# Performance work log

Measured on AMD Instinct MI355X. Metric: run time of the kernel, lower is better.

## Reference

```python
import jax, jax.numpy as jnp
import numpy as np

H = 128      # hidden_dim
HEADS = 4
HD = H // HEADS
B, S, D, A, I = 64, 512, 64, 3, 13


def layernorm(x, g, b, eps=1e-5):
    m = x.mean(-1, keepdims=True)
    v = ((x - m) ** 2).mean(-1, keepdims=True)
    return g * (x - m) / jnp.sqrt(v + eps) + b


def setup_inputs() -> dict:
    key = jax.random.key(0)
    ks = jax.random.split(key, 12)
    rn = lambda k, shp, s=0.05: jax.random.normal(k, shp, jnp.float32) * s
    return {
        "x": jax.random.normal(ks[0], (B, S, D), jnp.float32),
        "info": jax.random.normal(ks[1], (B, I), jnp.float32),
        "W_cell": rn(ks[2], (4 * H, D + H)), "b_cell": jnp.zeros(4 * H, jnp.float32),
        "Wqkv": rn(ks[3], (3 * H, H)), "bqkv": jnp.zeros(3 * H, jnp.float32),
        "Wo": rn(ks[4], (H, H)), "bo": jnp.zeros(H, jnp.float32),
        "ln_g": jnp.ones(H, jnp.float32), "ln_b": jnp.zeros(H, jnp.float32),
        "Wa1": rn(ks[5], (128, H + I)), "ba1": jnp.zeros(128, jnp.float32),
        "lna_g": jnp.ones(128, jnp.float32), "lna_b": jnp.zeros(128, jnp.float32),
        "Wa2": rn(ks[6], (A, 128)), "ba2": jnp.zeros(A, jnp.float32),
        "Wc1": rn(ks[7], (128, H + I)), "bc1": jnp.zeros(128, jnp.float32),
        "lnc_g": jnp.ones(128, jnp.float32), "lnc_b": jnp.zeros(128, jnp.float32),
        "Wc2": rn(ks[8], (1, 128)), "bc2": jnp.zeros(1, jnp.float32),
    }


def reference(x, info, W_cell, b_cell, Wqkv, bqkv, Wo, bo, ln_g, ln_b,
              Wa1, ba1, lna_g, lna_b, Wa2, ba2, Wc1, bc1, lnc_g, lnc_b, Wc2, bc2):
    Bx, Sx, _ = x.shape
    h0 = jnp.zeros((Bx, H), x.dtype)
    c0 = jnp.zeros((Bx, H), x.dtype)
    n0 = jnp.ones((Bx, H), x.dtype)

    def step(carry, xt):
        h, c, n = carry
        gates = jnp.concatenate([xt, h], -1) @ W_cell.T + b_cell
        i, f, o, z = jnp.split(gates, 4, axis=-1)
        i = jnp.exp(jnp.clip(i, -5.0, 5.0))
        f = jnp.exp(jnp.clip(f, -5.0, 5.0))
        c = jnp.clip(f * c + i * jnp.tanh(z), -1e6, 1e6)
        n = jnp.clip(f * n + i, 1e-6, 1e6)
        h = jnp.nan_to_num(jax.nn.sigmoid(o) * (c / n), nan=0.0, posinf=0.0, neginf=0.0)
        return (h, c, n), h

    _, hs = jax.lax.scan(step, (h0, c0, n0), jnp.swapaxes(x, 0, 1))  # (S,B,H)
    seq_h = jnp.swapaxes(hs, 0, 1)  # (B,S,H)

    # MultiheadAttention (self-attn, batch_first, shared in_proj)
    qkv = seq_h @ Wqkv.T + bqkv
    q, k, v = jnp.split(qkv, 3, -1)
    split_heads = lambda t: t.reshape(Bx, Sx, HEADS, HD).transpose(0, 2, 1, 3)
    q, k, v = split_heads(q), split_heads(k), split_heads(v)
    scores = jnp.einsum('bhqd,bhkd->bhqk', q, k) / np.sqrt(HD).astype(np.float32)
    attn = jax.nn.softmax(scores, axis=-1)
    av = jnp.einsum('bhqk,bhkd->bhqd', attn, v).transpose(0, 2, 1, 3).reshape(Bx, Sx, H)
    attn_out = av @ Wo.T + bo
    context = layernorm(seq_h + attn_out, ln_g, ln_b).mean(axis=1)  # (B,H)

    comb = jnp.concatenate([context, info], -1)  # (B, H+I)
    action_probs = jax.nn.softmax(
        jax.nn.relu(layernorm(comb @ Wa1.T + ba1, lna_g, lna_b)) @ Wa2.T + ba2, axis=-1)
    value = jax.nn.relu(layernorm(comb @ Wc1.T + bc1, lnc_g, lnc_b)) @ Wc2.T + bc2
    return (action_probs, value)
```

## Files before the change

kernel.cpp:

```cpp
#include <hip/hip_runtime.h>

typedef unsigned short ushort_t;
typedef unsigned int uint_t;

__device__ __forceinline__ float bflo(uint_t u){ union{uint_t i;float f;}v; v.i=u<<16; return v.f; }
__device__ __forceinline__ float bfhi(uint_t u){ union{uint_t i;float f;}v; v.i=u&0xffff0000u; return v.f; }
__device__ __forceinline__ float bfu(ushort_t u){ union{uint_t i;float f;}v; v.i=((uint_t)u)<<16; return v.f; }
__device__ __forceinline__ ushort_t f2b(float f){
  union{float f;uint_t i;}v; v.f=f;
  uint_t r = v.i + 0x7fffu + ((v.i>>16)&1u);
  return (ushort_t)(r>>16);
}
__device__ __forceinline__ void ld8bf(const ushort_t* p, float* w){
  uint4 u = *(const uint4*)p;
  w[0]=bflo(u.x); w[1]=bfhi(u.x); w[2]=bflo(u.y); w[3]=bfhi(u.y);
  w[4]=bflo(u.z); w[5]=bfhi(u.z); w[6]=bflo(u.w); w[7]=bfhi(u.w);
}
__device__ __forceinline__ void cvt8(uint4 u, float* d){
  d[0]=bflo(u.x); d[1]=bfhi(u.x); d[2]=bflo(u.y); d[3]=bfhi(u.y);
  d[4]=bflo(u.z); d[5]=bfhi(u.z); d[6]=bflo(u.w); d[7]=bfhi(u.w);
}
__device__ __forceinline__ float ldin(const void* p, size_t i, int isbf){
  return isbf ? bfu(((const ushort_t*)p)[i]) : ((const float*)p)[i];
}
__device__ __forceinline__ float rlane(float v, int l){
  return __uint_as_float(__builtin_amdgcn_readlane(__float_as_uint(v), l));
}

#define DOT128(acc, Wv, Bv) { float s0_=0.f,s1_=0.f,s2_=0.f,s3_=0.f; \
  _Pragma("unroll") \
  for (int k_=0;k_<128;k_+=4){ float4 h4_ = *(const float4*)&(Bv)[k_]; \
    s0_ += (Wv)[k_]*h4_.x; s1_ += (Wv)[k_+1]*h4_.y; \
    s2_ += (Wv)[k_+2]*h4_.z; s3_ += (Wv)[k_+3]*h4_.w; } \
  acc += (s0_+s1_)+(s2_+s3_); }
#define DOT64A(acc, Wv, Bv) { float s0_=0.f,s1_=0.f,s2_=0.f,s3_=0.f; \
  _Pragma("unroll") \
  for (int k_=0;k_<64;k_+=4){ float4 h4_ = *(const float4*)&(Bv)[k_]; \
    s0_ += (Wv)[k_]*h4_.x; s1_ += (Wv)[k_+1]*h4_.y; \
    s2_ += (Wv)[k_+2]*h4_.z; s3_ += (Wv)[k_+3]*h4_.w; } \
  acc += (s0_+s1_)+(s2_+s3_); }

typedef __attribute__((ext_vector_type(8))) short bf16x8;
typedef __attribute__((ext_vector_type(8))) _Float16 f16x8;
typedef __attribute__((ext_vector_type(4))) float f32x4;
__device__ __forceinline__ bf16x8 bcast8(uint4 u){ return __builtin_bit_cast(bf16x8, u); }
__device__ __forceinline__ f16x8  hcast8(uint4 u){ return __builtin_bit_cast(f16x8, u); }
__device__ __forceinline__ bf16x8 cvt8bf(const float* p){
  float4 a = *(const float4*)p; float4 b = *(const float4*)(p+4);
  uint4 u;
  u.x = (uint_t)f2b(a.x) | ((uint_t)f2b(a.y)<<16);
  u.y = (uint_t)f2b(a.z) | ((uint_t)f2b(a.w)<<16);
  u.z = (uint_t)f2b(b.x) | ((uint_t)f2b(b.y)<<16);
  u.w = (uint_t)f2b(b.z) | ((uint_t)f2b(b.w)<<16);
  return bcast8(u);
}
__device__ __forceinline__ void cvt8hl(const float* p, bf16x8* hi, bf16x8* lo){
  float v[8];
  *(float4*)&v[0] = *(const float4*)p;
  *(float4*)&v[4] = *(const float4*)(p+4);
  ushort_t h[8], l[8];
  #pragma unroll
  for (int j=0;j<8;++j){ h[j] = f2b(v[j]); l[j] = f2b(v[j] - bfu(h[j])); }
  uint4 uh = { (uint_t)h[0]|((uint_t)h[1]<<16), (uint_t)h[2]|((uint_t)h[3]<<16),
               (uint_t)h[4]|((uint_t)h[5]<<16), (uint_t)h[6]|((uint_t)h[7]<<16) };
  uint4 ul = { (uint_t)l[0]|((uint_t)l[1]<<16), (uint_t)l[2]|((uint_t)l[3]<<16),
               (uint_t)l[4]|((uint_t)l[5]<<16), (uint_t)l[6]|((uint_t)l[7]<<16) };
  *hi = bcast8(uh); *lo = bcast8(ul);
}
__device__ __forceinline__ ushort_t f2h(float f){
  _Float16 h = (_Float16)f;
  return __builtin_bit_cast(ushort_t, h);
}
__device__ __forceinline__ float h2f(ushort_t u){
  _Float16 h = __builtin_bit_cast(_Float16, u);
  return (float)h;
}

__global__ void k_detect(const uint_t* __restrict__ lng_raw, int* __restrict__ flag){
  if (threadIdx.x == 0) *flag = (lng_raw[0] == 0x3F803F80u) ? 1 : 0;
}

__global__ __launch_bounds__(256) void k_cvtw(const float* __restrict__ Wq,
    const float* __restrict__ Wo, const float* __restrict__ Wc,
    ushort_t* __restrict__ wqb, ushort_t* __restrict__ wob,
    ushort_t* __restrict__ wxh, ushort_t* __restrict__ wxl,
    ushort_t* __restrict__ whf, ushort_t* __restrict__ whl,
    const int* __restrict__ flag){
  if (*flag == 1) return;
  int i = blockIdx.x*256 + threadIdx.x;
  if (i < 12288){
    float4 f = ((const float4*)Wq)[i];
    uint2 u = { (uint_t)f2b(f.x) | ((uint_t)f2b(f.y)<<16),
                (uint_t)f2b(f.z) | ((uint_t)f2b(f.w)<<16) };
    ((uint2*)wqb)[i] = u;
  } else if (i < 16384){
    int k = i - 12288;
    float4 f = ((const float4*)Wo)[k];
    uint2 u = { (uint_t)f2b(f.x) | ((uint_t)f2b(f.y)<<16),
                (uint_t)f2b(f.z) | ((uint_t)f2b(f.w)<<16) };
    ((uint2*)wob)[k] = u;
  } else if (i < 24576){
    int k = i - 16384;
    int j = k >> 4, kq = (k & 15)*4;
    float4 f = *(const float4*)(Wc + (size_t)j*192 + kq);
    ushort_t h0=f2b(f.x), h1=f2b(f.y), h2=f2b(f.z), h3=f2b(f.w);
    ushort_t l0=f2b(f.x-bfu(h0)), l1=f2b(f.y-bfu(h1));
    ushort_t l2=f2b(f.z-bfu(h2)), l3=f2b(f.w-bfu(h3));
    ((uint2*)(wxh + (size_t)j*64 + kq))[0] = { (uint_t)h0|((uint_t)h1<<16), (uint_t)h2|((uint_t)h3<<16) };
    ((uint2*)(wxl + (size_t)j*64 + kq))[0] = { (uint_t)l0|((uint_t)l1<<16), (uint_t)l2|((uint_t)l3<<16) };
  } else if (i < 32768){
    int k2 = i - 24576;
    int j = k2 >> 4, kc = (k2 & 15)*8;
    const float* src = Wc + (size_t)j*192 + 64 + kc;
    ushort_t hh[8], ll[8];
    #pragma unroll
    for (int q=0;q<8;++q){
      hh[q] = f2h(src[q]);
      ll[q] = f2h(src[q] - h2f(hh[q]));
    }
    uint4 uh = { (uint_t)hh[0]|((uint_t)hh[1]<<16), (uint_t)hh[2]|((uint_t)hh[3]<<16),
                 (uint_t)hh[4]|((uint_t)hh[5]<<16), (uint_t)hh[6]|((uint_t)hh[7]<<16) };
    uint4 ul = { (uint_t)ll[0]|((uint_t)ll[1]<<16), (uint_t)ll[2]|((uint_t)ll[3]<<16),
                 (uint_t)ll[4]|((uint_t)ll[5]<<16), (uint_t)ll[6]|((uint_t)ll[7]<<16) };
    *(uint4*)(whf + (size_t)j*136 + kc) = uh;
    *(uint4*)(whl + (size_t)j*128 + kc) = ul;
  }
}

__global__ __launch_bounds__(256) void k_gx_bf(const void* __restrict__ x,
    const void* __restrict__ Wc, const void* __restrict__ bc,
    float* __restrict__ gx, const int* __restrict__ flag){
  if (*flag == 0) return;
  __shared__ float xs[2048];
  int row0 = blockIdx.x*32, t = threadIdx.x;
  {
    uint4 u = ((const uint4*)((const ushort_t*)x + (size_t)row0*64))[t];
    cvt8(u, &xs[t*8]);
  }
  __syncthreads();
  for (int pass=0; pass<2; ++pass){
    int j = t + pass*256;
    float w[64];
    const ushort_t* wr = (const ushort_t*)Wc + (size_t)j*192;
    #pragma unroll
    for (int q=0;q<8;q++) ld8bf(wr + 8*q, &w[8*q]);
    float bj = bfu(((const ushort_t*)bc)[j]);
    for (int s=0;s<32;++s){
      float acc = bj;
      DOT64A(acc, w, &xs[s*64]);
      gx[(size_t)(row0+s)*512 + j] = acc;
    }
  }
}

__global__ __launch_bounds__(256) void k_gx_f32(const float* __restrict__ x,
    const float* __restrict__ bc,
    const ushort_t* __restrict__ wxh, const ushort_t* __restrict__ wxl,
    float* __restrict__ gx, const int* __restrict__ flag){
  if (*flag == 1) return;
  int t = threadIdx.x, lane = t & 63, wave = t >> 6;
  int l16 = lane & 15, quad = lane >> 4;
  int rowb = blockIdx.x*64 + wave*16;
  const float* xp = x + (size_t)(rowb + l16)*64;
  bf16x8 xh0, xl0, xh1, xl1;
  cvt8hl(xp + quad*8,      &xh0, &xl0);
  cvt8hl(xp + 32 + quad*8, &xh1, &xl1);
  int r0 = rowb + quad*4;
  for (int ct=0; ct<32; ++ct){
    int j = ct*16 + l16;
    const ushort_t* bh = wxh + (size_t)j*64 + quad*8;
    const ushort_t* bl = wxl + (size_t)j*64 + quad*8;
    bf16x8 wh0 = bcast8(*(const uint4*)(bh));
    bf16x8 wh1 = bcast8(*(const uint4*)(bh + 32));
    bf16x8 wl0 = bcast8(*(const uint4*)(bl));
    bf16x8 wl1 = bcast8(*(const uint4*)(bl + 32));
    f32x4 acc = {0.f,0.f,0.f,0.f};
    acc = __builtin_amdgcn_mfma_f32_16x16x32_bf16(xh0, wh0, acc, 0,0,0);
    acc = __builtin_amdgcn_mfma_f32_16x16x32_bf16(xh1, wh1, acc, 0,0,0);
    acc = __builtin_amdgcn_mfma_f32_16x16x32_bf16(xh0, wl0, acc, 0,0,0);
    acc = __builtin_amdgcn_mfma_f32_16x16x32_bf16(xh1, wl1, acc, 0,0,0);
    acc = __builtin_amdgcn_mfma_f32_16x16x32_bf16(xl0, wh0, acc, 0,0,0);
    acc = __builtin_amdgcn_mfma_f32_16x16x32_bf16(xl1, wh1, acc, 0,0,0);
    float bj = bc[j];
    #pragma unroll
    for (int r=0;r<4;++r)
      gx[(size_t)(r0+r)*512 + j] = acc[r] + bj;
  }
}

__global__ __attribute__((amdgpu_flat_work_group_size(1024,1024), amdgpu_waves_per_eu(4,4)))
void k_rec_hl(const ushort_t* __restrict__ whf,
    const ushort_t* __restrict__ whl,
    const float* __restrict__ gx, float* __restrict__ seq_h,
    const int* __restrict__ flag){
  if (*flag == 1) return;
  int b = blockIdx.x, t = threadIdx.x;
  int lane = t & 63, wv = t >> 6, l16 = lane & 15, quad = lane >> 4;
  __shared__ ushort_t wlds[512*136];
  __shared__ float gs[512];
  __shared__ ushort_t hh[128], hl[128];
  {
    const uint4* src = (const uint4*)whf;
    uint4* dst = (uint4*)wlds;
    for (int i=t; i<8704; i+=1024) dst[i] = src[i];
  }
  if (t < 128){ hh[t] = (ushort_t)0; hl[t] = (ushort_t)0; }
  const float* gxb = gx + (size_t)b*512*512;
  float g0=0.f,g1=0.f,g2=0.f,g3=0.f;
  float c = 0.f, n = 1.f;
  if (t < 128){
    g0 = gxb[t]; g1 = gxb[128+t]; g2 = gxb[256+t]; g3 = gxb[384+t];
  }
  float* shout = seq_h + (size_t)b*512*128;
  __syncthreads();
  const int ct0 = 2*wv, ct1 = 2*wv+1;
  const ushort_t* w0 = wlds + (ct0*16 + l16)*136 + quad*8;
  const ushort_t* w1 = wlds + (ct1*16 + l16)*136 + quad*8;
  const ushort_t* v0 = whl + (size_t)(ct0*16 + l16)*128 + quad*8;
  const ushort_t* v1 = whl + (size_t)(ct1*16 + l16)*128 + quad*8;
  uint4 U00 = *(const uint4*)(w0),    U01 = *(const uint4*)(w0+32);
  uint4 U02 = *(const uint4*)(w0+64), U03 = *(const uint4*)(w0+96);
  uint4 U10 = *(const uint4*)(w1),    U11 = *(const uint4*)(w1+32);
  uint4 U12 = *(const uint4*)(w1+64), U13 = *(const uint4*)(w1+96);
  uint4 V00 = *(const uint4*)(v0),    V01 = *(const uint4*)(v0+32);
  uint4 V02 = *(const uint4*)(v0+64), V03 = *(const uint4*)(v0+96);
  uint4 V10 = *(const uint4*)(v1),    V11 = *(const uint4*)(v1+32);
  uint4 V12 = *(const uint4*)(v1+64), V13 = *(const uint4*)(v1+96);
#define UPIN(U) asm volatile("" : "+v"(U.x), "+v"(U.y), "+v"(U.z), "+v"(U.w));
  UPIN(U00) UPIN(U01) UPIN(U02) UPIN(U03)
  UPIN(U10) UPIN(U11) UPIN(U12) UPIN(U13)
  UPIN(V00) UPIN(V01) UPIN(V02) UPIN(V03)
  UPIN(V10) UPIN(V11) UPIN(V12) UPIN(V13)
#undef UPIN
  const uint4 zero4 = {0u,0u,0u,0u};
  for (int ts=0; ts<512; ++ts){
    uint4 a0 = zero4, a1 = zero4, a2 = zero4, a3 = zero4;
    if (l16 == 0){
      a0 = *(const uint4*)&hh[quad*8];
      a1 = *(const uint4*)&hh[32+quad*8];
      a2 = *(const uint4*)&hh[64+quad*8];
      a3 = *(const uint4*)&hh[96+quad*8];
    } else if (l16 == 1){
      a0 = *(const uint4*)&hl[quad*8];
      a1 = *(const uint4*)&hl[32+quad*8];
      a2 = *(const uint4*)&hl[64+quad*8];
      a3 = *(const uint4*)&hl[96+quad*8];
    }
    f16x8 A0 = hcast8(a0), A1 = hcast8(a1), A2 = hcast8(a2), A3 = hcast8(a3);
    f32x4 s0 = {0.f,0.f,0.f,0.f}, s1 = {0.f,0.f,0.f,0.f};
    s0 = __builtin_amdgcn_mfma_f32_16x16x32_f16(A0, hcast8(U00), s0, 0,0,0);
    s1 = __builtin_amdgcn_mfma_f32_16x16x32_f16(A0, hcast8(U10), s1, 0,0,0);
    s0 = __builtin_amdgcn_mfma_f32_16x16x32_f16(A1, hcast8(U01), s0, 0,0,0);
    s1 = __builtin_amdgcn_mfma_f32_16x16x32_f16(A1, hcast8(U11), s1, 0,0,0);
    s0 = __builtin_amdgcn_mfma_f32_16x16x32_f16(A2, hcast8(U02), s0, 0,0,0);
    s1 = __builtin_amdgcn_mfma_f32_16x16x32_f16(A2, hcast8(U12), s1, 0,0,0);
    s0 = __builtin_amdgcn_mfma_f32_16x16x32_f16(A3, hcast8(U03), s0, 0,0,0);
    s1 = __builtin_amdgcn_mfma_f32_16x16x32_f16(A3, hcast8(U13), s1, 0,0,0);
    s0 = __builtin_amdgcn_mfma_f32_16x16x32_f16(A0, hcast8(V00), s0, 0,0,0);
    s1 = __builtin_amdgcn_mfma_f32_16x16x32_f16(A0, hcast8(V10), s1, 0,0,0);
    s0 = __builtin_amdgcn_mfma_f32_16x16x32_f16(A1, hcast8(V01), s0, 0,0,0);
    s1 = __builtin_amdgcn_mfma_f32_16x16x32_f16(A1, hcast8(V11), s1, 0,0,0);
    s0 = __builtin_amdgcn_mfma_f32_16x16x32_f16(A2, hcast8(V02), s0, 0,0,0);
    s1 = __builtin_amdgcn_mfma_f32_16x16x32_f16(A2, hcast8(V12), s1, 0,0,0);
    s0 = __builtin_amdgcn_mfma_f32_16x16x32_f16(A3, hcast8(V03), s0, 0,0,0);
    s1 = __builtin_amdgcn_mfma_f32_16x16x32_f16(A3, hcast8(V13), s1, 0,0,0);
    if (quad == 0){
      gs[ct0*16 + l16] = s0[0] + s0[1];
      gs[ct1*16 + l16] = s1[0] + s1[1];
    }
    __syncthreads();
    if (t < 128){
      float gi = gs[t]     + g0;
      float gf = gs[128+t] + g1;
      float go = gs[256+t] + g2;
      float gz = gs[384+t] + g3;
      if (ts+1 < 512){
        const float* gn = gxb + (size_t)(ts+1)*512;
        g0 = gn[t]; g1 = gn[128+t]; g2 = gn[256+t]; g3 = gn[384+t];
      }
      float ii = __expf(fminf(fmaxf(gi,-5.f),5.f));
      float ff = __expf(fminf(fmaxf(gf,-5.f),5.f));
      float e2 = __expf(2.f*gz);
      float zt = 1.f - 2.f/(e2+1.f);
      c = fminf(fmaxf(ff*c + ii*zt, -1e6f), 1e6f);
      n = fminf(fmaxf(ff*n + ii, 1e-6f), 1e6f);
      float oo = 1.f/(1.f+__expf(-go));
      float h = oo*(c/n);
      if (!isfinite(h)) h = 0.f;
      shout[(size_t)ts*128 + t] = h;
      ushort_t hhi = f2h(h);
      hh[t] = hhi;
      hl[t] = f2h(h - h2f(hhi));
    }
    __syncthreads();
  }
}

__global__ __launch_bounds__(1024, 4) void k_rec_bf(const void* __restrict__ Wc,
    const float* __restrict__ gx, float* __restrict__ seq_h,
    const int* __restrict__ flag){
  if (*flag == 0) return;
  int b = blockIdx.x, t = threadIdx.x;
  int lane = t & 63, j = t & 511, half = t >> 9;
  __shared__ float ps[1024];
  __shared__ float hs[128];
  uint_t wu[32];
  {
    const uint4* wp = (const uint4*)((const ushort_t*)Wc + (size_t)j*192 + 64 + 64*half);
    #pragma unroll
    for (int q=0;q<8;q++){ uint4 u = wp[q];
      wu[4*q]=u.x; wu[4*q+1]=u.y; wu[4*q+2]=u.z; wu[4*q+3]=u.w; }
  }
  const float* gxb = gx + (size_t)b*512*512;
  float g0=0.f, g1=0.f;
  if (half==0){ g0 = gxb[j]; g1 = gxb[512 + j]; }
  float hreg = 0.f;
  float c = 0.f, n = 1.f;
  float* shout = seq_h + (size_t)b*512*128;
  for (int ts=0; ts<512; ++ts){
    float a0, a1=0.f, a2=0.f, a3=0.f;
    if (half==0){
      a0 = g0; g0 = g1;
      g1 = (ts+2 < 512) ? gxb[(size_t)(ts+2)*512 + j] : 0.f;
    } else a0 = 0.f;
    #pragma unroll
    for (int kk=0; kk<32; kk+=2){
      float h0v = rlane(hreg, 2*kk),   h1v = rlane(hreg, 2*kk+1);
      float h2v = rlane(hreg, 2*kk+2), h3v = rlane(hreg, 2*kk+3);
      a0 = fmaf(bflo(wu[kk]),   h0v, a0);
      a1 = fmaf(bfhi(wu[kk]),   h1v, a1);
      a2 = fmaf(bflo(wu[kk+1]), h2v, a2);
      a3 = fmaf(bfhi(wu[kk+1]), h3v, a3);
    }
    ps[t] = (a0+a1)+(a2+a3);
    __syncthreads();
    if (t < 128){
      float gi = ps[t]     + ps[512+t];
      float gf = ps[128+t] + ps[640+t];
      float go = ps[256+t] + ps[768+t];
      float gz = ps[384+t] + ps[896+t];
      float ii = __expf(fminf(fmaxf(gi,-5.f),5.f));
      float ff = __expf(fminf(fmaxf(gf,-5.f),5.f));
      float e2 = __expf(2.f*gz);
      float zt = 1.f - 2.f/(e2+1.f);
      c = fminf(fmaxf(ff*c + ii*zt, -1e6f), 1e6f);
      n = fminf(fmaxf(ff*n + ii, 1e-6f), 1e6f);
      float oo = 1.f/(1.f+__expf(-go));
      float h = oo*(c/n);
      if (!isfinite(h)) h = 0.f;
      hs[t] = h;
      shout[(size_t)ts*128 + t] = h;
    }
    __syncthreads();
    hreg = hs[(half<<6) | lane];
  }
}

__global__ __launch_bounds__(512) void k_rec_inl(const void* __restrict__ x,
    const void* __restrict__ Wc, const void* __restrict__ bc,
    float* __restrict__ seq_h, const int* __restrict__ flag){
  int isbf = *flag;
  int b = blockIdx.x, j = threadIdx.x;
  __shared__ float hs[128];
  __shared__ float gs[512];
  __shared__ float xr[4][64];
  float w[128], wx[64];
  if (isbf){
    const ushort_t* wr = (const ushort_t*)Wc + (size_t)j*192;
    #pragma unroll
    for (int q=0;q<8;q++)  ld8bf(wr + 8*q, &wx[8*q]);
    #pragma unroll
    for (int q=0;q<16;q++) ld8bf(wr + 64 + 8*q, &w[8*q]);
  } else {
    const float* wr = (const float*)Wc + (size_t)j*192;
    #pragma unroll
    for (int q=0;q<16;q++){ float4 f=*(const float4*)(wr+4*q);
      wx[4*q]=f.x; wx[4*q+1]=f.y; wx[4*q+2]=f.z; wx[4*q+3]=f.w; }
    #pragma unroll
    for (int q=0;q<32;q++){ float4 f=*(const float4*)(wr+64+4*q);
      w[4*q]=f.x; w[4*q+1]=f.y; w[4*q+2]=f.z; w[4*q+3]=f.w; }
  }
  float bj = ldin(bc, j, isbf);
  float c = 0.f, n = 1.f;
  if (j < 128) hs[j] = 0.f;
  if (j < 128){
    int r = j>>6, k = j&63;
    xr[r][k] = ldin(x, ((size_t)b*512 + r)*64 + k, isbf);
  }
  __syncthreads();
  for (int t=0; t<512; ++t){
    const float* xt = xr[t&3];
    float acc = bj;
    DOT64A(acc, wx, xt);
    DOT128(acc, w, hs);
    gs[j] = acc;
    __syncthreads();
    if (j < 128){
      float gi=gs[j], gf=gs[128+j], go=gs[256+j], gz=gs[384+j];
      float ii = __expf(fminf(fmaxf(gi,-5.f),5.f));
      float ff = __expf(fminf(fmaxf(gf,-5.f),5.f));
      float e2 = __expf(2.f*gz);
      float zt = 1.f - 2.f/(e2+1.f);
      c = fminf(fmaxf(ff*c + ii*zt, -1e6f), 1e6f);
      n = fminf(fmaxf(ff*n + ii, 1e-6f), 1e6f);
      float oo = 1.f/(1.f+__expf(-go));
      float h = oo*(c/n);
      if (!isfinite(h)) h = 0.f;
      hs[j] = h;
      seq_h[((size_t)b*512 + t)*128 + j] = h;
    } else if (j >= 448 && (t+2) < 512){
      int k = j & 63;
      xr[(t+2)&3][k] = ldin(x, ((size_t)b*512 + (t+2))*64 + k, isbf);
    }
    __syncthreads();
  }
}

__global__ __launch_bounds__(256) void k_qkv(const float* __restrict__ seq_h,
    const void* __restrict__ Wq, const void* __restrict__ bq,
    const ushort_t* __restrict__ wqb,
    ushort_t* __restrict__ qkv, const int* __restrict__ flag){
  int isbf = *flag;
  int row0 = blockIdx.x*32, t = threadIdx.x;
  if (isbf){
    __shared__ float hsb[4096];
    {
      const float4* hp = (const float4*)(seq_h + (size_t)row0*128);
      #pragma unroll
      for (int i=t;i<1024;i+=256) ((float4*)hsb)[i] = hp[i];
    }
    __syncthreads();
    for (int pass=0; pass<2; ++pass){
      int j = (pass==0) ? t : 256 + t;
      if (j >= 384) break;
      float w[128];
      const ushort_t* wr = (const ushort_t*)Wq + (size_t)j*128;
      #pragma unroll
      for (int q=0;q<16;q++) ld8bf(wr + 8*q, &w[8*q]);
      float bj = bfu(((const ushort_t*)bq)[j]);
      for (int s=0;s<32;++s){
        float acc = bj;
        DOT128(acc, w, &hsb[s*128]);
        qkv[(size_t)(row0+s)*384 + j] = f2b(acc);
      }
    }
  } else {
    int lane = t & 63, wave = t >> 6, l16 = lane & 15, quad = lane >> 4;
    int rt = wave & 1, chalf = wave >> 1;
    int rowg = row0 + rt*16 + l16;
    const float* hp = seq_h + (size_t)rowg*128 + quad*8;
    bf16x8 A0 = cvt8bf(hp);
    bf16x8 A1 = cvt8bf(hp + 32);
    bf16x8 A2 = cvt8bf(hp + 64);
    bf16x8 A3 = cvt8bf(hp + 96);
    int rbase = row0 + rt*16 + quad*4;
    for (int ci=0; ci<12; ++ci){
      int ct = chalf*12 + ci;
      int col = ct*16 + l16;
      const ushort_t* wb = wqb + (size_t)col*128 + quad*8;
      f32x4 acc = {0.f,0.f,0.f,0.f};
      acc = __builtin_amdgcn_mfma_f32_16x16x32_bf16(A0, bcast8(*(const uint4*)(wb)),      acc, 0,0,0);
      acc = __builtin_amdgcn_mfma_f32_16x16x32_bf16(A1, bcast8(*(const uint4*)(wb + 32)), acc, 0,0,0);
      acc = __builtin_amdgcn_mfma_f32_16x16x32_bf16(A2, bcast8(*(const uint4*)(wb + 64)), acc, 0,0,0);
      acc = __builtin_amdgcn_mfma_f32_16x16x32_bf16(A3, bcast8(*(const uint4*)(wb + 96)), acc, 0,0,0);
      float bj = ((const float*)bq)[col];
      #pragma unroll
      for (int r=0;r<4;++r)
        qkv[(size_t)(rbase+r)*384 + col] = f2b(acc[r] + bj);
    }
  }
}

#define AROW4(OP) OP(0) OP(1) OP(2) OP(3)
__global__ __launch_bounds__(512) void k_attn(const ushort_t* __restrict__ qkv,
    ushort_t* __restrict__ av){
  int b = blockIdx.x >> 2, h = blockIdx.x & 3;
  int t = threadIdx.x, lane = t & 63, wave = t >> 6;
  int l16 = lane & 15, quad = lane >> 4;
  __shared__ ushort_t Vt[32*512];
  __shared__ ushort_t Pl[8*16*64];
  const ushort_t* base = qkv + (size_t)b*512*384 + h*32;
  {
    const ushort_t* vr = base + (size_t)t*384 + 256;
    ushort_t tmp[32];
    *(uint4*)&tmp[0]  = *(const uint4*)(vr);
    *(uint4*)&tmp[8]  = *(const uint4*)(vr+8);
    *(uint4*)&tmp[16] = *(const uint4*)(vr+16);
    *(uint4*)&tmp[24] = *(const uint4*)(vr+24);
    #pragma unroll
    for (int d=0; d<32; ++d) Vt[d*512 + t] = tmp[d];
  }
  __syncthreads();
  ushort_t* Pw = Pl + wave*16*64;
  const float scale = 0.17677669529663687f;
  for (int q4=0; q4<4; ++q4){
    int qt = wave + q4*8;
    bf16x8 qa;
    { uint4 u = *(const uint4*)(base + (size_t)(qt*16 + l16)*384 + quad*8);
      qa = bcast8(u); }
    f32x4 O0 = {0.f,0.f,0.f,0.f}, O1 = {0.f,0.f,0.f,0.f};
    float m0=-1e30f,m1=-1e30f,m2=-1e30f,m3=-1e30f;
    float l0=0.f,l1=0.f,l2=0.f,l3=0.f;
    for (int ch=0; ch<8; ++ch){
      f32x4 S0,S1,S2,S3;
      {
        const ushort_t* kb = base + 128 + quad*8;
        uint4 u0 = *(const uint4*)(kb + (size_t)(ch*64 +  0 + l16)*384);
        uint4 u1 = *(const uint4*)(kb + (size_t)(ch*64 + 16 + l16)*384);
        uint4 u2 = *(const uint4*)(kb + (size_t)(ch*64 + 32 + l16)*384);
        uint4 u3 = *(const uint4*)(kb + (size_t)(ch*64 + 48 + l16)*384);
        f32x4 z = {0.f,0.f,0.f,0.f};
        S0 = __builtin_amdgcn_mfma_f32_16x16x32_bf16(qa, bcast8(u0), z, 0,0,0);
        S1 = __builtin_amdgcn_mfma_f32_16x16x32_bf16(qa, bcast8(u1), z, 0,0,0);
        S2 = __builtin_amdgcn_mfma_f32_16x16x32_bf16(qa, bcast8(u2), z, 0,0,0);
        S3 = __builtin_amdgcn_mfma_f32_16x16x32_bf16(qa, bcast8(u3), z, 0,0,0);
      }
#define CMAX(r) float c##r = fmaxf(fmaxf(S0[r],S1[r]), fmaxf(S2[r],S3[r])) * scale; \
      c##r = fmaxf(c##r, __shfl_xor(c##r,1)); c##r = fmaxf(c##r, __shfl_xor(c##r,2)); \
      c##r = fmaxf(c##r, __shfl_xor(c##r,4)); c##r = fmaxf(c##r, __shfl_xor(c##r,8)); \
      float M##r = fmaxf(m##r, c##r); float al##r = __expf(m##r - M##r); \
      m##r = M##r; O0[r] *= al##r; O1[r] *= al##r; l##r *= al##r;
      AROW4(CMAX)
#undef CMAX
#define PEXP(r) float ps##r; { \
      float p0 = __expf(S0[r]*scale - m##r); \
      float p1 = __expf(S1[r]*scale - m##r); \
      float p2 = __expf(S2[r]*scale - m##r); \
      float p3 = __expf(S3[r]*scale - m##r); \
      ps##r = (p0+p1)+(p2+p3); \
      Pw[(quad*4+(r))*64 +  0 + l16] = f2b(p0); \
      Pw[(quad*4+(r))*64 + 16 + l16] = f2b(p1); \
      Pw[(quad*4+(r))*64 + 32 + l16] = f2b(p2); \
      Pw[(quad*4+(r))*64 + 48 + l16] = f2b(p3); }
      AROW4(PEXP)
#undef PEXP
#define PSUM(r) ps##r += __shfl_xor(ps##r,1); ps##r += __shfl_xor(ps##r,2); \
      ps##r += __shfl_xor(ps##r,4); ps##r += __shfl_xor(ps##r,8); l##r += ps##r;
      AROW4(PSUM)
#undef PSUM
      asm volatile("s_waitcnt lgkmcnt(0)" ::: "memory");
      bf16x8 pa0, pa1;
      { uint4 u = *(const uint4*)&Pw[l16*64 + quad*8];      pa0 = bcast8(u); }
      { uint4 u = *(const uint4*)&Pw[l16*64 + 32 + quad*8]; pa1 = bcast8(u); }
      {
        uint4 v0 = *(const uint4*)&Vt[(l16)*512    + ch*64 + quad*8];
        uint4 v1 = *(const uint4*)&Vt[(l16)*512    + ch*64 + 32 + quad*8];
        uint4 v2 = *(const uint4*)&Vt[(16+l16)*512 + ch*64 + quad*8];
        uint4 v3 = *(const uint4*)&Vt[(16+l16)*512 + ch*64 + 32 + quad*8];
        O0 = __builtin_amdgcn_mfma_f32_16x16x32_bf16(pa0, bcast8(v0), O0, 0,0,0);
        O0 = __builtin_amdgcn_mfma_f32_16x16x32_bf16(pa1, bcast8(v1), O0, 0,0,0);
        O1 = __builtin_amdgcn_mfma_f32_16x16x32_bf16(pa0, bcast8(v2), O1, 0,0,0);
        O1 = __builtin_amdgcn_mfma_f32_16x16x32_bf16(pa1, bcast8(v3), O1, 0,0,0);
      }
    }
#define OST(r) { float iv = 1.f/l##r; int row = qt*16 + quad*4 + (r); \
      ushort_t* op = av + (size_t)(b*512 + row)*128 + h*32; \
      op[l16]      = f2b(O0[r]*iv); \
      op[16 + l16] = f2b(O1[r]*iv); }
    AROW4(OST)
#undef OST
  }
}

__global__ __launch_bounds__(256) void k_ctx(const ushort_t* __restrict__ av,
    const float* __restrict__ seq_h, const void* __restrict__ Wo,
    const void* __restrict__ bo_, const void* __restrict__ lng,
    const void* __restrict__ lnb, const ushort_t* __restrict__ wob,
    float* __restrict__ partial, const int* __restrict__ flag){
  int isbf = *flag;
  __shared__ float rs[4096];
  __shared__ float mrow[32], srow[32];
  __shared__ float halfsum[128];
  int row0 = blockIdx.x*32, t = threadIdx.x;
  int j = t & 127, sh = t >> 7;
  if (isbf){
    __shared__ float avs[4096];
    {
      const uint4* ap = (const uint4*)(av + (size_t)row0*128);
      for (int i=t;i<512;i+=256) cvt8(ap[i], &avs[i*8]);
    }
    __syncthreads();
    float w[128];
    const ushort_t* wr = (const ushort_t*)Wo + (size_t)j*128;
    #pragma unroll
    for (int q=0;q<16;q++) ld8bf(wr + 8*q, &w[8*q]);
    float bj = bfu(((const ushort_t*)bo_)[j]);
    for (int si=0; si<16; ++si){
      int s = sh*16 + si;
      float acc = bj;
      DOT128(acc, w, &avs[s*128]);
      rs[s*128+j] = acc + seq_h[(size_t)(row0+s)*128 + j];
    }
  } else {
    int lane = t & 63, wave = t >> 6, l16 = lane & 15, quad = lane >> 4;
    int rt = wave & 1, chalf = wave >> 1;
    int rowg = row0 + rt*16 + l16;
    const ushort_t* ap = av + (size_t)rowg*128 + quad*8;
    bf16x8 A0 = bcast8(*(const uint4*)(ap));
    bf16x8 A1 = bcast8(*(const uint4*)(ap + 32));
    bf16x8 A2 = bcast8(*(const uint4*)(ap + 64));
    bf16x8 A3 = bcast8(*(const uint4*)(ap + 96));
    int rl0 = rt*16 + quad*4;
    for (int ci=0; ci<4; ++ci){
      int ct = chalf*4 + ci;
      int col = ct*16 + l16;
      const ushort_t* wb = wob + (size_t)col*128 + quad*8;
      f32x4 acc = {0.f,0.f,0.f,0.f};
      acc = __builtin_amdgcn_mfma_f32_16x16x32_bf16(A0, bcast8(*(const uint4*)(wb)),      acc, 0,0,0);
      acc = __builtin_amdgcn_mfma_f32_16x16x32_bf16(A1, bcast8(*(const uint4*)(wb + 32)), acc, 0,0,0);
      acc = __builtin_amdgcn_mfma_f32_16x16x32_bf16(A2, bcast8(*(const uint4*)(wb + 64)), acc, 0,0,0);
      acc = __builtin_amdgcn_mfma_f32_16x16x32_bf16(A3, bcast8(*(const uint4*)(wb + 96)), acc, 0,0,0);
      float bj2 = ((const float*)bo_)[col];
      #pragma unroll
      for (int r=0;r<4;++r){
        int rl = rl0 + r;
        rs[rl*128 + col] = acc[r] + bj2 + seq_h[(size_t)(row0+rl)*128 + col];
      }
    }
  }
  __syncthreads();
  {
    int rr = t>>3, part = t&7;
    float vals[16], sm = 0.f;
    #pragma unroll
    for (int k2=0;k2<16;k2++){ vals[k2] = rs[rr*128 + part + 8*k2]; sm += vals[k2]; }
    sm += __shfl_xor(sm,1); sm += __shfl_xor(sm,2); sm += __shfl_xor(sm,4);
    float mean = sm*(1.f/128.f);
    float vv = 0.f;
    #pragma unroll
    for (int k2=0;k2<16;k2++){ float d = vals[k2]-mean; vv += d*d; }
    vv += __shfl_xor(vv,1); vv += __shfl_xor(vv,2); vv += __shfl_xor(vv,4);
    if (part==0){ mrow[rr]=mean; srow[rr]=rsqrtf(vv*(1.f/128.f)+1e-5f); }
  }
  __syncthreads();
  float g = ldin(lng, j, isbf), bb = ldin(lnb, j, isbf);
  float accs = 0.f;
  for (int si=0; si<16; ++si){
    int s = sh*16 + si;
    accs += g*(rs[s*128+j]-mrow[s])*srow[s] + bb;
  }
  if (sh==0) halfsum[j] = accs;
  __syncthreads();
  if (sh==1){
    int bidx = row0>>9, tile = (row0>>5)&15;
    partial[((size_t)bidx*16 + tile)*128 + j] = halfsum[j] + accs;
  }
}

__global__ __launch_bounds__(128) void k_head(const float* __restrict__ partial,
    const void* __restrict__ info,
    const void* Wa1, const void* ba1, const void* lnag, const void* lnab,
    const void* Wa2, const void* ba2,
    const void* Wc1, const void* bc1, const void* lncg, const void* lncb,
    const void* Wc2, const void* bc2, void* __restrict__ out,
    const int* __restrict__ flag){
  int isbf = *flag;
  int b = blockIdx.x, t = threadIdx.x;
  __shared__ float comb[144];
  __shared__ float red[128];
  __shared__ float uu[128];
  float s = 0.f;
  #pragma unroll
  for (int i=0;i<16;i++) s += partial[((size_t)b*16+i)*128 + t];
  comb[t] = s*(1.f/512.f);
  if (t < 13) comb[128+t] = ldin(info, (size_t)b*13+t, isbf);
  __syncthreads();
  for (int br=0; br<2; ++br){
    const void* W1 = br ? Wc1 : Wa1;
    const void* b1 = br ? bc1 : ba1;
    const void* lg_ = br ? lncg : lnag;
    const void* lb_ = br ? lncb : lnab;
    float a = ldin(b1, t, isbf);
    for (int k=0;k<141;k++) a += ldin(W1, (size_t)t*141+k, isbf)*comb[k];
    red[t] = a; __syncthreads();
    for (int st=64; st>0; st>>=1){ if (t<st) red[t]+=red[t+st]; __syncthreads(); }
    float mean = red[0]*(1.f/128.f);
    __syncthreads();
    float d = a - mean;
    red[t] = d*d; __syncthreads();
    for (int st=64; st>0; st>>=1){ if (t<st) red[t]+=red[t+st]; __syncthreads(); }
    float rstd = rsqrtf(red[0]*(1.f/128.f)+1e-5f);
    __syncthreads();
    float u = ldin(lg_, t, isbf)*d*rstd + ldin(lb_, t, isbf);
    uu[t] = fmaxf(u, 0.f);
    __syncthreads();
    if (br==0){
      if (t < 3){
        float lg2 = ldin(ba2, t, isbf);
        for (int k=0;k<128;k++) lg2 += ldin(Wa2, (size_t)t*128+k, isbf)*uu[k];
        red[t] = lg2;
      }
      __syncthreads();
      if (t==0){
        float mx = fmaxf(red[0], fmaxf(red[1], red[2]));
        float e0=__expf(red[0]-mx), e1=__expf(red[1]-mx), e2=__expf(red[2]-mx);
        float inv = 1.f/(e0+e1+e2);
        if (isbf){
          ushort_t* o = (ushort_t*)out;
          o[b*3+0]=f2b(e0*inv); o[b*3+1]=f2b(e1*inv); o[b*3+2]=f2b(e2*inv);
        } else {
          float* o = (float*)out;
          o[b*3+0]=e0*inv; o[b*3+1]=e1*inv; o[b*3+2]=e2*inv;
        }
      }
      __syncthreads();
    } else {
      if (t==0){
        float v = ldin(bc2, 0, isbf);
        for (int k=0;k<128;k++) v += ldin(Wc2, k, isbf)*uu[k];
        if (isbf) ((ushort_t*)out)[192 + b] = f2b(v);
        else      ((float*)out)[192 + b] = v;
      }
    }
  }
}

extern "C" void kernel_launch(void* const* d_in, const int* in_sizes, int n_in,
                              void* d_out, int out_size, void* d_ws, size_t ws_size,
                              hipStream_t stream){
  const void* x    = d_in[0];
  const void* info = d_in[1];
  const void* Wcell= d_in[2];
  const void* bcell= d_in[3];
  const void* Wqkv = d_in[4];
  const void* bqkv = d_in[5];
  const void* Wo   = d_in[6];
  const void* bo   = d_in[7];
  const void* lng  = d_in[8];
  const void* lnb  = d_in[9];
  const void* Wa1  = d_in[10];
  const void* ba1  = d_in[11];
  const void* lnag = d_in[12];
  const void* lnab = d_in[13];
  const void* Wa2  = d_in[14];
  const void* ba2  = d_in[15];
  const void* Wc1  = d_in[16];
  const void* bc1  = d_in[17];
  const void* lncg = d_in[18];
  const void* lncb = d_in[19];
  const void* Wc2  = d_in[20];
  const void* bc2  = d_in[21];

  char* ws = (char*)d_ws;
  const int bigws = (ws_size >= ((size_t)82<<20)) ? 1 : 0;
  float*    seqh = (float*)   ws;
  float*    gxf  = (float*)   (ws + ((size_t)16<<20));
  ushort_t* qkv  = (ushort_t*)(ws + ((size_t)16<<20));
  ushort_t* av   = (ushort_t*)(ws + ((size_t)40<<20));
  float*    part = (float*)   (ws + ((size_t)48<<20));
  int*      flag = bigws ? (int*)(ws + ((size_t)80<<20))
                         : (int*)(ws + ((size_t)48<<20) + (512<<10));
  ushort_t* wqb  = (ushort_t*)(ws + ((size_t)80<<20) + (1<<20));
  ushort_t* wob  = wqb + 384*128;
  ushort_t* wxh  = wob + 128*128;
  ushort_t* wxl  = wxh + 512*64;
  ushort_t* whf  = wxl + 512*64;
  ushort_t* whl  = whf + 512*136;

  k_detect<<<1, 64, 0, stream>>>((const uint_t*)lng, flag);
  if (bigws){
    k_cvtw  <<< 128, 256, 0, stream>>>((const float*)Wqkv, (const float*)Wo,
                                       (const float*)Wcell, wqb, wob, wxh, wxl, whf, whl, flag);
    k_gx_bf <<<1024, 256, 0, stream>>>(x, Wcell, bcell, gxf, flag);
    k_gx_f32<<< 512, 256, 0, stream>>>((const float*)x, (const float*)bcell,
                                       wxh, wxl, gxf, flag);
    k_rec_bf <<< 64, 1024, 0, stream>>>(Wcell, gxf, seqh, flag);
    k_rec_hl <<< 64, 1024, 0, stream>>>(whf, whl, gxf, seqh, flag);
  } else {
    k_rec_inl<<<64, 512, 0, stream>>>(x, Wcell, bcell, seqh, flag);
    k_cvtw  <<< 128, 256, 0, stream>>>((const float*)Wqkv, (const float*)Wo,
                                       (const float*)Wcell, wqb, wob, wxh, wxl, whf, whl, flag);
  }
  k_qkv <<<1024, 256, 0, stream>>>(seqh, Wqkv, bqkv, wqb, qkv, flag);
  k_attn<<< 256, 512, 0, stream>>>(qkv, av);
  k_ctx <<<1024, 256, 0, stream>>>(av, seqh, Wo, bo, lng, lnb, wob, part, flag);
  k_head<<<  64, 128, 0, stream>>>(part, info, Wa1, ba1, lnag, lnab, Wa2, ba2,
                                   Wc1, bc1, lncg, lncb, Wc2, bc2, d_out, flag);
}
```

Baseline: 761.9 us.

## Halve recurrence block to 512 threads with four MFMA tiles per wave

The hl recurrence kernel now runs 8 waves per block instead of 16, and each wave computes four 16-column gate tiles instead of two, keeping twice as many weight fragments pinned in registers. The hi/lo h buffers are merged into one zero-padded LDS array, so every lane does an unconditional vector load instead of branching on the lane index. The aim is cheaper per-step __syncthreads across fewer waves and less divergent LDS loading. The cost is a longer serial chain of MFMAs per wave and higher register pressure, with waves_per_eu lowered to 2 to make room.

```diff
diff --git a/kernel.cpp b/kernel.cpp
--- a/kernel.cpp
+++ b/kernel.cpp
@@ -188,7 +188,7 @@
   }
 }
 
-__global__ __attribute__((amdgpu_flat_work_group_size(1024,1024), amdgpu_waves_per_eu(4,4)))
+__global__ __attribute__((amdgpu_flat_work_group_size(512,512), amdgpu_waves_per_eu(2,2)))
 void k_rec_hl(const ushort_t* __restrict__ whf,
     const ushort_t* __restrict__ whl,
     const float* __restrict__ gx, float* __restrict__ seq_h,
@@ -198,13 +198,13 @@
   int lane = t & 63, wv = t >> 6, l16 = lane & 15, quad = lane >> 4;
   __shared__ ushort_t wlds[512*136];
   __shared__ float gs[512];
-  __shared__ ushort_t hh[128], hl[128];
+  __shared__ ushort_t hz[384];
   {
     const uint4* src = (const uint4*)whf;
     uint4* dst = (uint4*)wlds;
-    for (int i=t; i<8704; i+=1024) dst[i] = src[i];
-  }
-  if (t < 128){ hh[t] = (ushort_t)0; hl[t] = (ushort_t)0; }
+    for (int i=t; i<8704; i+=512) dst[i] = src[i];
+  }
+  if (t < 384) hz[t] = (ushort_t)0;
   const float* gxb = gx + (size_t)b*512*512;
   float g0=0.f,g1=0.f,g2=0.f,g3=0.f;
   float c = 0.f, n = 1.f;
@@ -213,60 +213,57 @@
   }
   float* shout = seq_h + (size_t)b*512*128;
   __syncthreads();
-  const int ct0 = 2*wv, ct1 = 2*wv+1;
-  const ushort_t* w0 = wlds + (ct0*16 + l16)*136 + quad*8;
-  const ushort_t* w1 = wlds + (ct1*16 + l16)*136 + quad*8;
-  const ushort_t* v0 = whl + (size_t)(ct0*16 + l16)*128 + quad*8;
-  const ushort_t* v1 = whl + (size_t)(ct1*16 + l16)*128 + quad*8;
-  uint4 U00 = *(const uint4*)(w0),    U01 = *(const uint4*)(w0+32);
-  uint4 U02 = *(const uint4*)(w0+64), U03 = *(const uint4*)(w0+96);
-  uint4 U10 = *(const uint4*)(w1),    U11 = *(const uint4*)(w1+32);
-  uint4 U12 = *(const uint4*)(w1+64), U13 = *(const uint4*)(w1+96);
-  uint4 V00 = *(const uint4*)(v0),    V01 = *(const uint4*)(v0+32);
-  uint4 V02 = *(const uint4*)(v0+64), V03 = *(const uint4*)(v0+96);
-  uint4 V10 = *(const uint4*)(v1),    V11 = *(const uint4*)(v1+32);
-  uint4 V12 = *(const uint4*)(v1+64), V13 = *(const uint4*)(v1+96);
+  const int c0 = 4*wv, c1 = 4*wv+1, c2 = 4*wv+2, c3 = 4*wv+3;
+  const ushort_t* w0 = wlds + (c0*16 + l16)*136 + quad*8;
+  const ushort_t* w1 = wlds + (c1*16 + l16)*136 + quad*8;
+  const ushort_t* w2 = wlds + (c2*16 + l16)*136 + quad*8;
+  const ushort_t* w3 = wlds + (c3*16 + l16)*136 + quad*8;
+  const ushort_t* p0 = whl + (size_t)(c0*16 + l16)*128 + quad*8;
+  const ushort_t* p1 = whl + (size_t)(c1*16 + l16)*128 + quad*8;
+  const ushort_t* p2 = whl + (size_t)(c2*16 + l16)*128 + quad*8;
+  const ushort_t* p3 = whl + (size_t)(c3*16 + l16)*128 + quad*8;
+#define BDECL(T, ptr) uint4 T##0 = *(const uint4*)(ptr), T##1 = *(const uint4*)((ptr)+32), \
+  T##2 = *(const uint4*)((ptr)+64), T##3 = *(const uint4*)((ptr)+96);
+  BDECL(U0, w0) BDECL(U1, w1) BDECL(U2, w2) BDECL(U3, w3)
+  BDECL(V0, p0) BDECL(V1, p1) BDECL(V2, p2) BDECL(V3, p3)
+#undef BDECL
 #define UPIN(U) asm volatile("" : "+v"(U.x), "+v"(U.y), "+v"(U.z), "+v"(U.w));
   UPIN(U00) UPIN(U01) UPIN(U02) UPIN(U03)
   UPIN(U10) UPIN(U11) UPIN(U12) UPIN(U13)
+  UPIN(U20) UPIN(U21) UPIN(U22) UPIN(U23)
+  UPIN(U30) UPIN(U31) UPIN(U32) UPIN(U33)
   UPIN(V00) UPIN(V01) UPIN(V02) UPIN(V03)
   UPIN(V10) UPIN(V11) UPIN(V12) UPIN(V13)
+  UPIN(V20) UPIN(V21) UPIN(V22) UPIN(V23)
+  UPIN(V30) UPIN(V31) UPIN(V32) UPIN(V33)
 #undef UPIN
-  const uint4 zero4 = {0u,0u,0u,0u};
+  const ushort_t* hzsel = hz + ((l16 < 2) ? l16*128 : 256) + quad*8;
   for (int ts=0; ts<512; ++ts){
-    uint4 a0 = zero4, a1 = zero4, a2 = zero4, a3 = zero4;
-    if (l16 == 0){
-      a0 = *(const uint4*)&hh[quad*8];
-      a1 = *(const uint4*)&hh[32+quad*8];
-      a2 = *(const uint4*)&hh[64+quad*8];
-      a3 = *(const uint4*)&hh[96+quad*8];
-    } else if (l16 == 1){
-      a0 = *(const uint4*)&hl[quad*8];
-      a1 = *(const uint4*)&hl[32+quad*8];
-      a2 = *(const uint4*)&hl[64+quad*8];
-      a3 = *(const uint4*)&hl[96+quad*8];
-    }
-    f16x8 A0 = hcast8(a0), A1 = hcast8(a1), A2 = hcast8(a2), A3 = hcast8(a3);
+    f16x8 A0 = hcast8(*(const uint4*)(hzsel));
+    f16x8 A1 = hcast8(*(const uint4*)(hzsel + 32));
+    f16x8 A2 = hcast8(*(const uint4*)(hzsel + 64));
+    f16x8 A3 = hcast8(*(const uint4*)(hzsel + 96));
     f32x4 s0 = {0.f,0.f,0.f,0.f}, s1 = {0.f,0.f,0.f,0.f};
-    s0 = __builtin_amdgcn_mfma_f32_16x16x32_f16(A0, hcast8(U00), s0, 0,0,0);
-    s1 = __builtin_amdgcn_mfma_f32_16x16x32_f16(A0, hcast8(U10), s1, 0,0,0);
-    s0 = __builtin_amdgcn_mfma_f32_16x16x32_f16(A1, hcast8(U01), s0, 0,0,0);
-    s1 = __builtin_amdgcn_mfma_f32_16x16x32_f16(A1, hcast8(U11), s1, 0,0,0);
-    s0 = __builtin_amdgcn_mfma_f32_16x16x32_f16(A2, hcast8(U02), s0, 0,0,0);
-    s1 = __builtin_amdgcn_mfma_f32_16x16x32_f16(A2, hcast8(U12), s1, 0,0,0);
-    s0 = __builtin_amdgcn_mfma_f32_16x16x32_f16(A3, hcast8(U03), s0, 0,0,0);
-    s1 = __builtin_amdgcn_mfma_f32_16x16x32_f16(A3, hcast8(U13), s1, 0,0,0);
-    s0 = __builtin_amdgcn_mfma_f32_16x16x32_f16(A0, hcast8(V00), s0, 0,0,0);
-    s1 = __builtin_amdgcn_mfma_f32_16x16x32_f16(A0, hcast8(V10), s1, 0,0,0);
-    s0 = __builtin_amdgcn_mfma_f32_16x16x32_f16(A1, hcast8(V01), s0, 0,0,0);
-    s1 = __builtin_amdgcn_mfma_f32_16x16x32_f16(A1, hcast8(V11), s1, 0,0,0);
-    s0 = __builtin_amdgcn_mfma_f32_16x16x32_f16(A2, hcast8(V02), s0, 0,0,0);
-    s1 = __builtin_amdgcn_mfma_f32_16x16x32_f16(A2, hcast8(V12), s1, 0,0,0);
-    s0 = __builtin_amdgcn_mfma_f32_16x16x32_f16(A3, hcast8(V03), s0, 0,0,0);
-    s1 = __builtin_amdgcn_mfma_f32_16x16x32_f16(A3, hcast8(V13), s1, 0,0,0);
+    f32x4 s2 = {0.f,0.f,0.f,0.f}, s3 = {0.f,0.f,0.f,0.f};
+#define TILE(sa, Uf, Vf) \
+    sa = __builtin_amdgcn_mfma_f32_16x16x32_f16(A0, hcast8(Uf##0), sa, 0,0,0); \
+    sa = __builtin_amdgcn_mfma_f32_16x16x32_f16(A1, hcast8(Uf##1), sa, 0,0,0); \
+    sa = __builtin_amdgcn_mfma_f32_16x16x32_f16(A2, hcast8(Uf##2), sa, 0,0,0); \
+    sa = __builtin_amdgcn_mfma_f32_16x16x32_f16(A3, hcast8(Uf##3), sa, 0,0,0); \
+    sa = __builtin_amdgcn_mfma_f32_16x16x32_f16(A0, hcast8(Vf##0), sa, 0,0,0); \
+    sa = __builtin_amdgcn_mfma_f32_16x16x32_f16(A1, hcast8(Vf##1), sa, 0,0,0); \
+    sa = __builtin_amdgcn_mfma_f32_16x16x32_f16(A2, hcast8(Vf##2), sa, 0,0,0); \
+    sa = __builtin_amdgcn_mfma_f32_16x16x32_f16(A3, hcast8(Vf##3), sa, 0,0,0);
+    TILE(s0, U0, V0)
+    TILE(s1, U1, V1)
+    TILE(s2, U2, V2)
+    TILE(s3, U3, V3)
+#undef TILE
     if (quad == 0){
-      gs[ct0*16 + l16] = s0[0] + s0[1];
-      gs[ct1*16 + l16] = s1[0] + s1[1];
+      gs[c0*16 + l16] = s0[0] + s0[1];
+      gs[c1*16 + l16] = s1[0] + s1[1];
+      gs[c2*16 + l16] = s2[0] + s2[1];
+      gs[c3*16 + l16] = s3[0] + s3[1];
     }
     __syncthreads();
     if (t < 128){
@@ -289,8 +286,8 @@
       if (!isfinite(h)) h = 0.f;
       shout[(size_t)ts*128 + t] = h;
       ushort_t hhi = f2h(h);
-      hh[t] = hhi;
-      hl[t] = f2h(h - h2f(hhi));
+      hz[t] = hhi;
+      hz[128+t] = f2h(h - h2f(hhi));
     }
     __syncthreads();
   }
@@ -765,7 +762,7 @@
     k_gx_f32<<< 512, 256, 0, stream>>>((const float*)x, (const float*)bcell,
                                        wxh, wxl, gxf, flag);
     k_rec_bf <<< 64, 1024, 0, stream>>>(Wcell, gxf, seqh, flag);
-    k_rec_hl <<< 64, 1024, 0, stream>>>(whf, whl, gxf, seqh, flag);
+    k_rec_hl <<< 64,  512, 0, stream>>>(whf, whl, gxf, seqh, flag);
   } else {
     k_rec_inl<<<64, 512, 0, stream>>>(x, Wcell, bcell, seqh, flag);
     k_cvtw  <<< 128, 256, 0, stream>>>((const float*)Wqkv, (const float*)Wo,
```

Measured after the change: 736.1 us. -3.4%, faster.
